# Performance work log

Hardware: AMD Instinct MI355X
Metric: run time of the kernel (lower is better)

The kernel has to match this reference:

```python
import jax, jax.numpy as jnp
import numpy as np

NUM_LEVELS = 16
LEVEL_DIM = 2
BASE_RES = 32
PER_LEVEL_SCALE = 2.0
TABLE_SIZE = 2 ** 19  # padded size of every level's table
RES = np.array([int(BASE_RES * PER_LEVEL_SCALE ** i) for i in range(NUM_LEVELS)], dtype=np.float32)
SIZES = np.minimum(RES.astype(np.float64) ** 3, TABLE_SIZE).astype(np.float32)  # true table sizes
NEAR, FAR, NUM_SAMPLES = 0.1, 1.5, 64
N_RAYS = 16384


def _xavier(key, fin, fout):
    lim = float(np.sqrt(6.0 / (fin + fout)))
    return jax.random.uniform(key, (fin, fout), jnp.float32, -lim, lim)


def setup_inputs() -> dict:
    key = jax.random.key(0)
    ks = jax.random.split(key, 12)
    rays_o = jax.random.uniform(ks[0], (N_RAYS, 3), jnp.float32, -0.5, 0.5)
    d = jax.random.normal(ks[1], (N_RAYS, 3), jnp.float32)
    rays_d = d / jnp.linalg.norm(d, axis=-1, keepdims=True)
    tables = jax.random.uniform(ks[2], (NUM_LEVELS, TABLE_SIZE, LEVEL_DIM), jnp.float32, -1e-4, 1e-4)
    return {
        'rays_o': rays_o, 'rays_d': rays_d, 'tables': tables,
        'Wg0': _xavier(ks[3], 32, 64), 'bg0': jnp.zeros((64,), jnp.float32),
        'Wg1': _xavier(ks[4], 64, 64), 'bg1': jnp.zeros((64,), jnp.float32),
        'Wd': _xavier(ks[5], 64, 16), 'bd': jnp.zeros((16,), jnp.float32),
        'Wc0': _xavier(ks[6], 24, 64), 'bc0': jnp.zeros((64,), jnp.float32),
        'Wc1': _xavier(ks[7], 64, 64), 'bc1': jnp.zeros((64,), jnp.float32),
        'Wc2': _xavier(ks[8], 64, 64), 'bc2': jnp.zeros((64,), jnp.float32),
        'Wch': _xavier(ks[9], 64, 3), 'bch': jnp.zeros((3,), jnp.float32),
    }


def _hash_encode(pts, tables):
    # pts: [N, S, 3] in roughly [-1, 1]; tables: [L, T, 2]
    res = jnp.asarray(RES)            # [L]
    sizes = jnp.asarray(SIZES)        # [L]
    scaled = (pts[..., None, :] + 1.0) / 2.0 * (res[:, None] - 1.0)     # [N,S,L,3]
    scaled = jnp.clip(scaled, 0.0, res[:, None] - 1.0)
    # torch computes the flat index in float then .long() (truncation), then clamps to table size
    idx_f = scaled[..., 0] * res * res + scaled[..., 1] * res + scaled[..., 2]  # [N,S,L]
    idx = jnp.minimum(idx_f, sizes - 1.0).astype(jnp.int32)
    feats = tables[jnp.arange(NUM_LEVELS)[None, None, :], idx]          # [N,S,L,2]
    return feats.reshape(feats.shape[:-2] + (NUM_LEVELS * LEVEL_DIM,))  # [N,S,32]


def _sh_encode(d):
    # degree-4 encoder in the source only ever builds 9 features
    x, y, z = d[..., 0], d[..., 1], d[..., 2]
    return jnp.stack([jnp.full_like(x, 0.5), x, y, z,
                      x * y, x * z, y * z, x * x - y * y, 3.0 * z * z - 1.0], axis=-1)  # [N,9]


def reference(rays_o, rays_d, tables, Wg0, bg0, Wg1, bg1, Wd, bd,
              Wc0, bc0, Wc1, bc1, Wc2, bc2, Wch, bch):
    n = rays_o.shape[0]
    # --- stratified-free (eval mode) sampling along rays ---
    t = jnp.linspace(0.0, 1.0, NUM_SAMPLES, dtype=jnp.float32)
    z_vals = jnp.broadcast_to(NEAR + (FAR - NEAR) * t, (n, NUM_SAMPLES))           # [N,S]
    pts = rays_o[:, None, :] + rays_d[:, None, :] * z_vals[..., None]              # [N,S,3]
    # --- LoDAwareNeRF forward ---
    feats = _hash_encode(pts, tables)                                              # [N,S,32]
    h = jax.nn.relu(feats @ Wg0 + bg0)
    h = jax.nn.relu(h @ Wg1 + bg1)
    geo = h @ Wd + bd                                                              # [N,S,16]
    density = jax.nn.softplus(geo[..., 0] - 1.0)                                   # [N,S]
    geo_feat = geo[..., 1:]                                                        # [N,S,15]
    dir_f = jnp.broadcast_to(_sh_encode(rays_d)[:, None, :], (n, NUM_SAMPLES, 9))  # [N,S,9]
    c = jnp.concatenate([geo_feat, dir_f], axis=-1)                                # [N,S,24]
    c = jax.nn.relu(c @ Wc0 + bc0)
    c = jax.nn.relu(c @ Wc1 + bc1)
    c = jax.nn.relu(c @ Wc2 + bc2)
    color = jax.nn.sigmoid(c @ Wch + bch)                                          # [N,S,3]
    # --- volume rendering compositing ---
    dists = z_vals[..., 1:] - z_vals[..., :-1]
    dists = jnp.concatenate([dists, jnp.full_like(dists[..., :1], 1e10)], axis=-1)
    dists = dists * jnp.linalg.norm(rays_d, axis=-1, keepdims=True)
    alpha = 1.0 - jnp.exp(-density * dists)                                        # [N,S]
    T = jnp.cumprod(1.0 - alpha + 1e-10, axis=-1)
    T = jnp.concatenate([jnp.ones_like(T[..., :1]), T[..., :-1]], axis=-1)
    weights = alpha * T                                                            # [N,S]
    rgb = jnp.sum(weights[..., None] * color, axis=-2)                             # [N,3]
    depth = jnp.sum(weights * z_vals, axis=-1)                                     # [N]
    acc = jnp.sum(weights, axis=-1)                                                # [N]
    return rgb, depth, acc, weights
```

## Files before the change

kernel.cpp:

```cpp
#include <hip/hip_runtime.h>
#include <hip/hip_bf16.h>
#include <math.h>

typedef float  f32x4 __attribute__((ext_vector_type(4)));
typedef short  s16x8 __attribute__((ext_vector_type(8)));
typedef unsigned int u32x2 __attribute__((ext_vector_type(2)));
typedef unsigned int u32x4 __attribute__((ext_vector_type(4)));

constexpr int kNRays = 16384;
constexpr int kOffDepth   = kNRays * 3;
constexpr int kOffAcc     = kOffDepth + kNRays;
constexpr int kOffWeights = kOffAcc + kNRays;

constexpr int kWg0 = 0;
constexpr int kWg1 = 2048;
constexpr int kWd  = 6144;
constexpr int kWc0 = 7168;
constexpr int kWc1 = 9216;
constexpr int kWc2 = 13312;
constexpr int kWch = 17408;
constexpr int kWsTotal = 18432;
constexpr int kPrepTotal = kWsTotal + 32;

__device__ __forceinline__ ushort f2bf(float x) {
    unsigned u = __float_as_uint(x);
    return (ushort)((u + 0x7FFFu + ((u >> 16) & 1u)) >> 16);
}
__device__ __forceinline__ unsigned pk2(float lo, float hi) {
    __hip_bfloat162 h = __float22bfloat162_rn(float2{lo, hi});
    return *reinterpret_cast<unsigned*>(&h);
}
__device__ __forceinline__ unsigned pk2r(float lo, float hi) {
    unsigned p = pk2(lo, hi), r;
    asm("v_pk_max_i16 %0, %1, 0" : "=v"(r) : "v"(p));
    return r;
}
__device__ __forceinline__ float sel4(float v0, float v1, float v2, float v3, int s) {
    float a = (s & 1) ? v1 : v0;
    float b = (s & 1) ? v3 : v2;
    return (s & 2) ? b : a;
}
template<int CTRL, int RMASK>
__device__ __forceinline__ float dpp_mul(float x) {
    int t = __builtin_amdgcn_update_dpp(0x3f800000, __float_as_int(x), CTRL, RMASK, 0xF, false);
    return x * __int_as_float(t);
}
template<int CTRL, int RMASK>
__device__ __forceinline__ float dpp_add(float x) {
    int t = __builtin_amdgcn_update_dpp(0, __float_as_int(x), CTRL, RMASK, 0xF, false);
    return x + __int_as_float(t);
}
__device__ __forceinline__ float dpp_sum64(float v) {
    v = dpp_add<0x111, 0xF>(v);
    v = dpp_add<0x112, 0xF>(v);
    v = dpp_add<0x114, 0xF>(v);
    v = dpp_add<0x118, 0xF>(v);
    v = dpp_add<0x142, 0xA>(v);
    v = dpp_add<0x143, 0xC>(v);
    return __int_as_float(__builtin_amdgcn_readlane(__float_as_int(v), 63));
}

__global__ __launch_bounds__(256) void prep_weights(
    const float* __restrict__ Wg0, const float* __restrict__ Wg1,
    const float* __restrict__ Wd,  const float* __restrict__ Wc0,
    const float* __restrict__ Wc1, const float* __restrict__ Wc2,
    const float* __restrict__ Wch, const float* __restrict__ bc0,
    const float* __restrict__ tables, ushort* __restrict__ ws)
{
    const int i = blockIdx.x * 256 + threadIdx.x;
    if (i >= kPrepTotal) return;
    if (i >= kWsTotal) {
        const int t = i - kWsTotal;
        if (t < 16) {
            const unsigned szm1 = (t == 0) ? 32767u : (t == 1) ? 262143u : 524287u;
            const float2 v = ((const float2*)tables)[((size_t)t << 19) + szm1];
            ((unsigned*)(ws + kWsTotal))[t] = pk2(v.x, v.y);
        }
        return;
    }
    if (i < kWg1) {
        const int r = i;
        const int e = r & 7, l = (r >> 3) & 63, mt = r >> 9;
        const int g = (l >> 4) & 3, c = l & 15;
        const int fr = 8 * (e >> 1) + 2 * g + (e & 1);
        ws[i] = f2bf(Wg0[fr * 64 + 16 * mt + c]);
        return;
    }
    const float* W; int FIN, FOUT, KT, base; bool dperm = false, c0bias = false;
    if (i < kWd)       { W = Wg1; FIN = 64; FOUT = 64; KT = 2; base = kWg1; }
    else if (i < kWc0) { W = Wd;  FIN = 64; FOUT = 16; KT = 2; base = kWd; dperm = true; }
    else if (i < kWc1) { W = Wc0; FIN = 24; FOUT = 64; KT = 1; base = kWc0; c0bias = true; }
    else if (i < kWc2) { W = Wc1; FIN = 64; FOUT = 64; KT = 2; base = kWc1; }
    else if (i < kWch) { W = Wc2; FIN = 64; FOUT = 64; KT = 2; base = kWc2; }
    else               { W = Wch; FIN = 64; FOUT = 3;  KT = 2; base = kWch; }
    const int r = i - base;
    const int e = r & 7, l = (r >> 3) & 63, t = r >> 9;
    const int kt = t % KT, mt = t / KT;
    const int k = kt * 32 + ((l >> 4) << 3) + e;
    int j = mt * 16 + (l & 15);
    if (dperm) j = (j == 15) ? 0 : j + 1;
    float w = 0.0f;
    if (k < FIN && j < FOUT) w = W[k * FOUT + j];
    if (c0bias && k == 24 && j < FOUT) w = bc0[j];
    ws[i] = f2bf(w);
}

template<int KT, bool HASBIAS>
__device__ __forceinline__ void layer64(ushort* __restrict__ Xw,
                                        const ushort* __restrict__ Aws,
                                        const float* __restrict__ bias,
                                        const int* rp, const int* wa,
                                        int g, int lane) {
    s16x8 B[KT][4];
#pragma unroll
    for (int kt = 0; kt < KT; ++kt)
#pragma unroll
        for (int nt = 0; nt < 4; ++nt)
            B[kt][nt] = *(const s16x8*)&Xw[rp[kt * 4 + nt]];
#pragma unroll
    for (int mt = 0; mt < 4; ++mt) {
        const s16x8 A0 = *(const s16x8*)&Aws[((mt * KT + 0) * 64 + lane) * 8];
        s16x8 A1;
        if constexpr (KT == 2) A1 = *(const s16x8*)&Aws[((mt * KT + 1) * 64 + lane) * 8];
        f32x4 b;
        if constexpr (HASBIAS) b = *(const f32x4*)(bias + mt * 16 + g * 4);
        else                   b = (f32x4){ 0.f, 0.f, 0.f, 0.f };
        f32x4 acc[4];
#pragma unroll
        for (int nt = 0; nt < 4; ++nt) {
            acc[nt] = __builtin_amdgcn_mfma_f32_16x16x32_bf16(A0, B[0][nt], b, 0, 0, 0);
            if constexpr (KT == 2)
                acc[nt] = __builtin_amdgcn_mfma_f32_16x16x32_bf16(A1, B[1][nt], acc[nt], 0, 0, 0);
        }
#pragma unroll
        for (int nt = 0; nt < 4; ++nt)
            *(u32x2*)&Xw[wa[mt * 4 + nt]] =
                (u32x2){ pk2r(acc[nt].x, acc[nt].y), pk2r(acc[nt].z, acc[nt].w) };
    }
}

__device__ __forceinline__ void layer16(const ushort* __restrict__ Xw,
                                        const ushort* __restrict__ Aws,
                                        const int* rp, int lane, f32x4 acc[4]) {
    const s16x8 A0 = *(const s16x8*)&Aws[(0 * 64 + lane) * 8];
    const s16x8 A1 = *(const s16x8*)&Aws[(1 * 64 + lane) * 8];
#pragma unroll
    for (int nt = 0; nt < 4; ++nt) {
        const s16x8 B0 = *(const s16x8*)&Xw[rp[0 * 4 + nt]];
        acc[nt] = __builtin_amdgcn_mfma_f32_16x16x32_bf16(A0, B0, acc[nt], 0, 0, 0);
        const s16x8 B1 = *(const s16x8*)&Xw[rp[1 * 4 + nt]];
        acc[nt] = __builtin_amdgcn_mfma_f32_16x16x32_bf16(A1, B1, acc[nt], 0, 0, 0);
    }
}

__device__ __forceinline__ void gather_j0(const float2* __restrict__ tb,
                                          float ox, float oy, float oz,
                                          float dx, float dy, float dz,
                                          int c16, int g, float2* __restrict__ f0) {
    const float step = 1.0f / 63.0f;
    const float tc = (float)c16 * step;
#pragma unroll
    for (int nt = 0; nt < 4; ++nt) {
        const float ts = tc + (float)nt * (16.0f / 63.0f);
        const float zs = fmaf(1.4f, ts, 0.1f);
        const float px = fmaf(dx, zs, ox), py = fmaf(dy, zs, oy), pz = fmaf(dz, zs, oz);
        const float res = (float)(32 << g);
        const float rm1 = res - 1.0f;
        const float hf = 0.5f * rm1;
        const float sx = __builtin_amdgcn_fmed3f(fmaf(px, hf, hf), 0.f, rm1);
        const float sy = __builtin_amdgcn_fmed3f(fmaf(py, hf, hf), 0.f, rm1);
        const float sz = __builtin_amdgcn_fmed3f(fmaf(pz, hf, hf), 0.f, rm1);
        const float idxf = fmaf(sx, res * res, fmaf(sy, res, sz));
        const float szm1 = (g == 0) ? 32767.f : (g == 1) ? 262143.f : 524287.f;
        const unsigned idx = (unsigned)(int)fminf(idxf, szm1);
        f0[nt] = tb[((unsigned)g << 19) + idx];
    }
}

__device__ __forceinline__ void make_B0(const float2* __restrict__ tb,
                                        float ox, float oy, float oz,
                                        float dx, float dy, float dz,
                                        bool allhi, const float2* __restrict__ f0,
                                        unsigned cj1, unsigned cj2, unsigned cj3,
                                        int c16, int g, s16x8* __restrict__ B0f) {
    const float step = 1.0f / 63.0f;
    const float tc = (float)c16 * step;
#pragma unroll
    for (int nt = 0; nt < 4; ++nt) {
        u32x4 val;
        val[0] = pk2(f0[nt].x, f0[nt].y);
        if (allhi) {
            val[1] = cj1; val[2] = cj2; val[3] = cj3;
        } else {
            const float ts = tc + (float)nt * (16.0f / 63.0f);
            const float zs = fmaf(1.4f, ts, 0.1f);
            const float px = fmaf(dx, zs, ox), py = fmaf(dy, zs, oy), pz = fmaf(dz, zs, oz);
#pragma unroll
            for (int j = 1; j < 4; ++j) {
                const int lv = 4 * j + g;
                const float res = (float)(32 << lv);
                const float rm1 = res - 1.0f;
                const float hf = 0.5f * rm1;
                const float sx = __builtin_amdgcn_fmed3f(fmaf(px, hf, hf), 0.f, rm1);
                const float sy = __builtin_amdgcn_fmed3f(fmaf(py, hf, hf), 0.f, rm1);
                const float sz = __builtin_amdgcn_fmed3f(fmaf(pz, hf, hf), 0.f, rm1);
                const float idxf = fmaf(sx, res * res, fmaf(sy, res, sz));
                const int idx = (int)fminf(idxf, 524287.f);
                unsigned u;
                if (__any(idx != 524287)) {
                    const float2 f2 = tb[((unsigned)lv << 19) + (unsigned)idx];
                    u = pk2(f2.x, f2.y);
                } else {
                    u = (j == 1) ? cj1 : (j == 2) ? cj2 : cj3;
                }
                val[j] = u;
            }
        }
        B0f[nt] = *(const s16x8*)&val;
    }
}

__device__ __forceinline__ void run_ray(ushort* __restrict__ Xw,
                                        const ushort* __restrict__ ws,
                                        const float* __restrict__ bg0,
                                        const float* __restrict__ bg1,
                                        const float* __restrict__ bc1,
                                        const float* __restrict__ bc2,
                                        const f32x4 bdv, const f32x4 bchv,
                                        const int* rp, const int* wa,
                                        int g, int c16, int lane,
                                        int ray, float dx, float dy, float dz,
                                        float z, float zn,
                                        const s16x8* __restrict__ B0f,
                                        float* __restrict__ out) {
#pragma unroll
    for (int mt = 0; mt < 4; ++mt) {
        const s16x8 A0 = *(const s16x8*)&ws[kWg0 + (mt * 64 + lane) * 8];
        const f32x4 b = *(const f32x4*)(bg0 + mt * 16 + g * 4);
        f32x4 acc[4];
#pragma unroll
        for (int nt = 0; nt < 4; ++nt)
            acc[nt] = __builtin_amdgcn_mfma_f32_16x16x32_bf16(A0, B0f[nt], b, 0, 0, 0);
#pragma unroll
        for (int nt = 0; nt < 4; ++nt)
            *(u32x2*)&Xw[wa[mt * 4 + nt]] =
                (u32x2){ pk2r(acc[nt].x, acc[nt].y), pk2r(acc[nt].z, acc[nt].w) };
    }

    layer64<2, true>(Xw, ws + kWg1, bg1, rp, wa, g, lane);

    f32x4 accd[4];
#pragma unroll
    for (int nt = 0; nt < 4; ++nt) accd[nt] = bdv;
    layer16(Xw, ws + kWd, rp, lane, accd);
    const float lgit = sel4(__shfl(accd[0].w, 48 + c16, 64),
                            __shfl(accd[1].w, 48 + c16, 64),
                            __shfl(accd[2].w, 48 + c16, 64),
                            __shfl(accd[3].w, 48 + c16, 64), g);
#pragma unroll
    for (int nt = 0; nt < 4; ++nt)
        *(u32x2*)&Xw[wa[nt]] = (u32x2){ pk2(accd[nt].x, accd[nt].y),
                                        pk2(accd[nt].z, accd[nt].w) };
    Xw[lane * 64 + 8 * (1 ^ (lane & 7)) + 7] = 0x3F00;
    {
        u32x4 w = { pk2(dx, dy), pk2(dz, dx * dy), pk2(dx * dz, dy * dz),
                    pk2(dx * dx - dy * dy, 3.f * dz * dz - 1.f) };
        *(u32x4*)&Xw[lane * 64 + 8 * (2 ^ (lane & 7))] = w;
    }
    {
        u32x4 w = { 0x00003F80u, 0u, 0u, 0u };
        *(u32x4*)&Xw[lane * 64 + 8 * (3 ^ (lane & 7))] = w;
    }

    layer64<1, false>(Xw, ws + kWc0, nullptr, rp, wa, g, lane);
    layer64<2, true >(Xw, ws + kWc1, bc1,     rp, wa, g, lane);
    layer64<2, true >(Xw, ws + kWc2, bc2,     rp, wa, g, lane);

    f32x4 accc[4];
#pragma unroll
    for (int nt = 0; nt < 4; ++nt) accc[nt] = bchv;
    layer16(Xw, ws + kWch, rp, lane, accc);
    const float lr  = sel4(__shfl(accc[0].x, c16, 64), __shfl(accc[1].x, c16, 64),
                           __shfl(accc[2].x, c16, 64), __shfl(accc[3].x, c16, 64), g);
    const float lgr = sel4(__shfl(accc[0].y, c16, 64), __shfl(accc[1].y, c16, 64),
                           __shfl(accc[2].y, c16, 64), __shfl(accc[3].y, c16, 64), g);
    const float lb  = sel4(__shfl(accc[0].z, c16, 64), __shfl(accc[1].z, c16, 64),
                           __shfl(accc[2].z, c16, 64), __shfl(accc[3].z, c16, 64), g);

    const float cr = 1.f / (1.f + __expf(-lr));
    const float cg = 1.f / (1.f + __expf(-lgr));
    const float cb = 1.f / (1.f + __expf(-lb));
    const float gx = lgit - 1.0f;
    const float density = fmaxf(gx, 0.f) + __logf(1.f + __expf(-fabsf(gx)));

    const float dnorm = sqrtf(dx * dx + dy * dy + dz * dz);
    float dist = (lane < 63) ? (zn - z) : 1e10f;
    dist *= dnorm;
    const float alpha = 1.0f - __expf(-density * dist);
    float f = 1.0f - alpha + 1e-10f;
    f = dpp_mul<0x111, 0xF>(f);
    f = dpp_mul<0x112, 0xF>(f);
    f = dpp_mul<0x114, 0xF>(f);
    f = dpp_mul<0x118, 0xF>(f);
    f = dpp_mul<0x142, 0xA>(f);
    f = dpp_mul<0x143, 0xC>(f);
    float T = __shfl_up(f, 1, 64);
    if (lane == 0) T = 1.0f;
    const float w = alpha * T;

    out[kOffWeights + ray * 64 + lane] = w;
    const float sr = dpp_sum64(w * cr);
    const float sg = dpp_sum64(w * cg);
    const float sb = dpp_sum64(w * cb);
    const float sd = dpp_sum64(w * z);
    const float sa = dpp_sum64(w);
    if (lane == 0) {
        out[ray * 3 + 0] = sr;
        out[ray * 3 + 1] = sg;
        out[ray * 3 + 2] = sb;
        out[kOffDepth + ray] = sd;
        out[kOffAcc + ray]   = sa;
    }
}

__global__ __launch_bounds__(256, 4) void nerf_mfma_kernel(
    const float* __restrict__ rays_o, const float* __restrict__ rays_d,
    const float* __restrict__ tables, const ushort* __restrict__ ws,
    const float* __restrict__ bg0, const float* __restrict__ bg1,
    const float* __restrict__ bd,  const float* __restrict__ bc1,
    const float* __restrict__ bc2, const float* __restrict__ bch,
    float* __restrict__ out)
{
    __shared__ __align__(16) ushort Xs[4 * 4096];
    const int tid  = threadIdx.x;
    const int wid  = tid >> 6;
    const int lane = tid & 63;
    const int c16  = lane & 15;
    const int g    = lane >> 4;
    ushort* Xw = Xs + wid * 4096;
    const int ray0 = blockIdx.x * 8 + wid * 2;

    const float step = 1.0f / 63.0f;
    const float z  = 0.1f + 1.4f * ((float)lane * step);
    const float zn = 0.1f + 1.4f * ((float)(lane + 1) * step);

    int rp[8], wa[16];
#pragma unroll
    for (int kt = 0; kt < 2; ++kt)
#pragma unroll
        for (int nt = 0; nt < 4; ++nt)
            rp[kt * 4 + nt] = (nt * 16 + c16) * 64 + 8 * ((kt * 4 + g) ^ (c16 & 7));
#pragma unroll
    for (int mt = 0; mt < 4; ++mt)
#pragma unroll
        for (int nt = 0; nt < 4; ++nt)
            wa[mt * 4 + nt] = (nt * 16 + c16) * 64
                            + 8 * ((2 * mt + (g >> 1)) ^ (c16 & 7)) + 4 * (g & 1);

    const unsigned* cstp = (const unsigned*)(ws + kWsTotal);
    const unsigned cj1 = cstp[4 + g], cj2 = cstp[8 + g], cj3 = cstp[12 + g];

    const f32x4 bdv = { bd[g * 4 + 1], bd[g * 4 + 2], bd[g * 4 + 3],
                        bd[(g == 3) ? 0 : g * 4 + 4] };
    const f32x4 bchv = (g == 0) ? (f32x4){ bch[0], bch[1], bch[2], 0.f }
                                : (f32x4){ 0.f, 0.f, 0.f, 0.f };

    const float2* __restrict__ tb = (const float2*)tables;

    const float oxA = rays_o[ray0 * 3 + 0], oyA = rays_o[ray0 * 3 + 1], ozA = rays_o[ray0 * 3 + 2];
    const float dxA = rays_d[ray0 * 3 + 0], dyA = rays_d[ray0 * 3 + 1], dzA = rays_d[ray0 * 3 + 2];
    float2 f0A[4];
    gather_j0(tb, oxA, oyA, ozA, dxA, dyA, dzA, c16, g, f0A);
    const bool hiA = fminf(fmaf(dxA, 0.1f, oxA), fmaf(dxA, 1.5f, oxA)) >= -0.98f;

    const int rayB = ray0 + 1;
    const float oxB = rays_o[rayB * 3 + 0], oyB = rays_o[rayB * 3 + 1], ozB = rays_o[rayB * 3 + 2];
    const float dxB = rays_d[rayB * 3 + 0], dyB = rays_d[rayB * 3 + 1], dzB = rays_d[rayB * 3 + 2];

    s16x8 B0f[4];
    make_B0(tb, oxA, oyA, ozA, dxA, dyA, dzA, hiA, f0A, cj1, cj2, cj3, c16, g, B0f);

    float2 f0B[4];
    gather_j0(tb, oxB, oyB, ozB, dxB, dyB, dzB, c16, g, f0B);
    const bool hiB = fminf(fmaf(dxB, 0.1f, oxB), fmaf(dxB, 1.5f, oxB)) >= -0.98f;

    run_ray(Xw, ws, bg0, bg1, bc1, bc2, bdv, bchv, rp, wa, g, c16, lane,
            ray0, dxA, dyA, dzA, z, zn, B0f, out);

    make_B0(tb, oxB, oyB, ozB, dxB, dyB, dzB, hiB, f0B, cj1, cj2, cj3, c16, g, B0f);
    run_ray(Xw, ws, bg0, bg1, bc1, bc2, bdv, bchv, rp, wa, g, c16, lane,
            rayB, dxB, dyB, dzB, z, zn, B0f, out);
}

extern "C" void kernel_launch(void* const* d_in, const int* in_sizes, int n_in,
                              void* d_out, int out_size, void* d_ws, size_t ws_size,
                              hipStream_t stream) {
    const float* rays_o = (const float*)d_in[0];
    const float* rays_d = (const float*)d_in[1];
    const float* tables = (const float*)d_in[2];
    const float* Wg0 = (const float*)d_in[3];
    const float* bg0 = (const float*)d_in[4];
    const float* Wg1 = (const float*)d_in[5];
    const float* bg1 = (const float*)d_in[6];
    const float* Wd  = (const float*)d_in[7];
    const float* bd  = (const float*)d_in[8];
    const float* Wc0 = (const float*)d_in[9];
    const float* bc0 = (const float*)d_in[10];
    const float* Wc1 = (const float*)d_in[11];
    const float* bc1 = (const float*)d_in[12];
    const float* Wc2 = (const float*)d_in[13];
    const float* bc2 = (const float*)d_in[14];
    const float* Wch = (const float*)d_in[15];
    const float* bch = (const float*)d_in[16];
    float* out = (float*)d_out;
    ushort* wsp = (ushort*)d_ws;

    prep_weights<<<dim3((kPrepTotal + 255) / 256), dim3(256), 0, stream>>>(
        Wg0, Wg1, Wd, Wc0, Wc1, Wc2, Wch, bc0, tables, wsp);

    nerf_mfma_kernel<<<dim3(kNRays / 8), dim3(256), 0, stream>>>(
        rays_o, rays_d, tables, wsp,
        bg0, bg1, bd, bc1, bc2, bch, out);
}
```

Before: 78.20 us.

## Interleave two rays per wave layer-by-layer with separate LDS buffers

Splits the per-ray MLP into stage functions and runs the two rays of each wave interleaved layer by layer, each with its own LDS scratch buffer. Both rays' hash gathers are issued together up front. The goal is to give the scheduler independent MFMA and LDS chains to overlap and to hide gather latency. In exchange it doubles LDS per wave and raises register pressure; blocks shrink to 128 threads with launch bounds of 3, which may lower occupancy.

```diff
diff --git a/kernel.cpp b/kernel.cpp
--- a/kernel.cpp
+++ b/kernel.cpp
@@ -220,19 +220,11 @@
     }
 }
 
-__device__ __forceinline__ void run_ray(ushort* __restrict__ Xw,
-                                        const ushort* __restrict__ ws,
-                                        const float* __restrict__ bg0,
-                                        const float* __restrict__ bg1,
-                                        const float* __restrict__ bc1,
-                                        const float* __restrict__ bc2,
-                                        const f32x4 bdv, const f32x4 bchv,
-                                        const int* rp, const int* wa,
-                                        int g, int c16, int lane,
-                                        int ray, float dx, float dy, float dz,
-                                        float z, float zn,
-                                        const s16x8* __restrict__ B0f,
-                                        float* __restrict__ out) {
+__device__ __forceinline__ void g0_layer(ushort* __restrict__ Xw,
+                                         const ushort* __restrict__ ws,
+                                         const float* __restrict__ bg0,
+                                         const int* wa, int g, int lane,
+                                         const s16x8* __restrict__ B0f) {
 #pragma unroll
     for (int mt = 0; mt < 4; ++mt) {
         const s16x8 A0 = *(const s16x8*)&ws[kWg0 + (mt * 64 + lane) * 8];
@@ -246,9 +238,14 @@
             *(u32x2*)&Xw[wa[mt * 4 + nt]] =
                 (u32x2){ pk2r(acc[nt].x, acc[nt].y), pk2r(acc[nt].z, acc[nt].w) };
     }
-
-    layer64<2, true>(Xw, ws + kWg1, bg1, rp, wa, g, lane);
-
+}
+
+__device__ __forceinline__ float d_section(ushort* __restrict__ Xw,
+                                           const ushort* __restrict__ ws,
+                                           const f32x4 bdv,
+                                           const int* rp, const int* wa,
+                                           int g, int c16, int lane,
+                                           float dx, float dy, float dz) {
     f32x4 accd[4];
 #pragma unroll
     for (int nt = 0; nt < 4; ++nt) accd[nt] = bdv;
@@ -271,11 +268,17 @@
         u32x4 w = { 0x00003F80u, 0u, 0u, 0u };
         *(u32x4*)&Xw[lane * 64 + 8 * (3 ^ (lane & 7))] = w;
     }
-
-    layer64<1, false>(Xw, ws + kWc0, nullptr, rp, wa, g, lane);
-    layer64<2, true >(Xw, ws + kWc1, bc1,     rp, wa, g, lane);
-    layer64<2, true >(Xw, ws + kWc2, bc2,     rp, wa, g, lane);
-
+    return lgit;
+}
+
+__device__ __forceinline__ void ch_render(const ushort* __restrict__ Xw,
+                                          const ushort* __restrict__ ws,
+                                          const f32x4 bchv,
+                                          const int* rp,
+                                          int g, int c16, int lane,
+                                          int ray, float dx, float dy, float dz,
+                                          float z, float zn, float lgit,
+                                          float* __restrict__ out) {
     f32x4 accc[4];
 #pragma unroll
     for (int nt = 0; nt < 4; ++nt) accc[nt] = bchv;
@@ -323,7 +326,7 @@
     }
 }
 
-__global__ __launch_bounds__(256, 4) void nerf_mfma_kernel(
+__global__ __launch_bounds__(128, 3) void nerf_mfma_kernel(
     const float* __restrict__ rays_o, const float* __restrict__ rays_d,
     const float* __restrict__ tables, const ushort* __restrict__ ws,
     const float* __restrict__ bg0, const float* __restrict__ bg1,
@@ -331,14 +334,16 @@
     const float* __restrict__ bc2, const float* __restrict__ bch,
     float* __restrict__ out)
 {
-    __shared__ __align__(16) ushort Xs[4 * 4096];
+    __shared__ __align__(16) ushort Xs[2 * 2 * 4096];
     const int tid  = threadIdx.x;
     const int wid  = tid >> 6;
     const int lane = tid & 63;
     const int c16  = lane & 15;
     const int g    = lane >> 4;
-    ushort* Xw = Xs + wid * 4096;
-    const int ray0 = blockIdx.x * 8 + wid * 2;
+    ushort* XwA = Xs + wid * 8192;
+    ushort* XwB = XwA + 4096;
+    const int rayA = blockIdx.x * 4 + wid * 2;
+    const int rayB = rayA + 1;
 
     const float step = 1.0f / 63.0f;
     const float z  = 0.1f + 1.4f * ((float)lane * step);
@@ -367,29 +372,41 @@
 
     const float2* __restrict__ tb = (const float2*)tables;
 
-    const float oxA = rays_o[ray0 * 3 + 0], oyA = rays_o[ray0 * 3 + 1], ozA = rays_o[ray0 * 3 + 2];
-    const float dxA = rays_d[ray0 * 3 + 0], dyA = rays_d[ray0 * 3 + 1], dzA = rays_d[ray0 * 3 + 2];
-    float2 f0A[4];
-    gather_j0(tb, oxA, oyA, ozA, dxA, dyA, dzA, c16, g, f0A);
-    const bool hiA = fminf(fmaf(dxA, 0.1f, oxA), fmaf(dxA, 1.5f, oxA)) >= -0.98f;
-
-    const int rayB = ray0 + 1;
+    const float oxA = rays_o[rayA * 3 + 0], oyA = rays_o[rayA * 3 + 1], ozA = rays_o[rayA * 3 + 2];
+    const float dxA = rays_d[rayA * 3 + 0], dyA = rays_d[rayA * 3 + 1], dzA = rays_d[rayA * 3 + 2];
     const float oxB = rays_o[rayB * 3 + 0], oyB = rays_o[rayB * 3 + 1], ozB = rays_o[rayB * 3 + 2];
     const float dxB = rays_d[rayB * 3 + 0], dyB = rays_d[rayB * 3 + 1], dzB = rays_d[rayB * 3 + 2];
 
-    s16x8 B0f[4];
-    make_B0(tb, oxA, oyA, ozA, dxA, dyA, dzA, hiA, f0A, cj1, cj2, cj3, c16, g, B0f);
-
-    float2 f0B[4];
+    float2 f0A[4], f0B[4];
+    gather_j0(tb, oxA, oyA, ozA, dxA, dyA, dzA, c16, g, f0A);
     gather_j0(tb, oxB, oyB, ozB, dxB, dyB, dzB, c16, g, f0B);
+    const bool hiA = fminf(fmaf(dxA, 0.1f, oxA), fmaf(dxA, 1.5f, oxA)) >= -0.98f;
     const bool hiB = fminf(fmaf(dxB, 0.1f, oxB), fmaf(dxB, 1.5f, oxB)) >= -0.98f;
 
-    run_ray(Xw, ws, bg0, bg1, bc1, bc2, bdv, bchv, rp, wa, g, c16, lane,
-            ray0, dxA, dyA, dzA, z, zn, B0f, out);
-
-    make_B0(tb, oxB, oyB, ozB, dxB, dyB, dzB, hiB, f0B, cj1, cj2, cj3, c16, g, B0f);
-    run_ray(Xw, ws, bg0, bg1, bc1, bc2, bdv, bchv, rp, wa, g, c16, lane,
-            rayB, dxB, dyB, dzB, z, zn, B0f, out);
+    s16x8 B0fA[4], B0fB[4];
+    make_B0(tb, oxA, oyA, ozA, dxA, dyA, dzA, hiA, f0A, cj1, cj2, cj3, c16, g, B0fA);
+    make_B0(tb, oxB, oyB, ozB, dxB, dyB, dzB, hiB, f0B, cj1, cj2, cj3, c16, g, B0fB);
+
+    g0_layer(XwA, ws, bg0, wa, g, lane, B0fA);
+    g0_layer(XwB, ws, bg0, wa, g, lane, B0fB);
+
+    layer64<2, true>(XwA, ws + kWg1, bg1, rp, wa, g, lane);
+    layer64<2, true>(XwB, ws + kWg1, bg1, rp, wa, g, lane);
+
+    const float lgitA = d_section(XwA, ws, bdv, rp, wa, g, c16, lane, dxA, dyA, dzA);
+    const float lgitB = d_section(XwB, ws, bdv, rp, wa, g, c16, lane, dxB, dyB, dzB);
+
+    layer64<1, false>(XwA, ws + kWc0, nullptr, rp, wa, g, lane);
+    layer64<1, false>(XwB, ws + kWc0, nullptr, rp, wa, g, lane);
+
+    layer64<2, true>(XwA, ws + kWc1, bc1, rp, wa, g, lane);
+    layer64<2, true>(XwB, ws + kWc1, bc1, rp, wa, g, lane);
+
+    layer64<2, true>(XwA, ws + kWc2, bc2, rp, wa, g, lane);
+    layer64<2, true>(XwB, ws + kWc2, bc2, rp, wa, g, lane);
+
+    ch_render(XwA, ws, bchv, rp, g, c16, lane, rayA, dxA, dyA, dzA, z, zn, lgitA, out);
+    ch_render(XwB, ws, bchv, rp, g, c16, lane, rayB, dxB, dyB, dzB, z, zn, lgitB, out);
 }
 
 extern "C" void kernel_launch(void* const* d_in, const int* in_sizes, int n_in,
@@ -418,7 +435,7 @@
     prep_weights<<<dim3((kPrepTotal + 255) / 256), dim3(256), 0, stream>>>(
         Wg0, Wg1, Wd, Wc0, Wc1, Wc2, Wch, bc0, tables, wsp);
 
-    nerf_mfma_kernel<<<dim3(kNRays / 8), dim3(256), 0, stream>>>(
+    nerf_mfma_kernel<<<dim3(kNRays / 4), dim3(128), 0, stream>>>(
         rays_o, rays_d, tables, wsp,
         bg0, bg1, bd, bc1, bc2, bch, out);
 }
```

New measurement: 79.24 us. Within noise of the previous version (+1.3%).
